# Kernel optimization log

Hardware: AMD Instinct MI355X
Metric: run time of the kernel (lower is better)

## Reference

```python
import jax, jax.numpy as jnp
import numpy as np

BN_EPS = 1e-5
N_IN, N_OUT = 200000, 400000
K, M, C_IN, C_OUT = 27, 100000, 64, 64


def setup_inputs() -> dict:
    key = jax.random.key(0)
    ks = jax.random.split(key, 4)
    x = jax.random.normal(ks[0], (N_IN, C_IN), dtype=jnp.float32)
    W = jax.random.normal(ks[1], (K, C_IN, C_OUT), dtype=jnp.float32) * 0.05
    gamma = jnp.ones((C_OUT,), dtype=jnp.float32)
    beta = jnp.zeros((C_OUT,), dtype=jnp.float32)
    in_idx = jax.random.randint(ks[2], (K, M), 0, N_IN, dtype=jnp.int32)
    out_idx = jax.random.randint(ks[3], (K, M), 0, N_OUT, dtype=jnp.int32)
    return {"x": x, "W": W, "gamma": gamma, "beta": beta,
            "in_idx": in_idx, "out_idx": out_idx, "n_out": N_OUT}


def reference(x, W, gamma, beta, in_idx, out_idx, n_out):
    # Sparse transposed conv via gather-GEMM-scatter over K kernel offsets.
    feats = x[in_idx]                               # [K, M, C_in] gather
    contrib = jnp.einsum('kmi,kio->kmo', feats, W)  # per-offset GEMM
    out = jnp.zeros((n_out, contrib.shape[-1]), dtype=x.dtype)
    out = out.at[out_idx.reshape(-1)].add(contrib.reshape(-1, contrib.shape[-1]))
    # BatchNorm (training-mode batch stats over all output points), gamma=1, beta=0 at init.
    mean = jnp.mean(out, axis=0)
    var = jnp.var(out, axis=0)
    y = (out - mean) * jax.lax.rsqrt(var + BN_EPS) * gamma + beta
    return jax.nn.relu(y)
```

## Files before the change

kernel.cpp:

```cpp
#include <hip/hip_runtime.h>
#include <hip/hip_bf16.h>

#define K_OFF 27
#define M_PTS 100000
#define C_CH 64
#define N_OUT_PTS 400000
#define BN_EPS 1e-5f
#define PTS_PER_WAVE 50

__device__ inline void pk_atomic_add_bf16(__hip_bfloat16* p, int bits) {
#if __has_builtin(__builtin_amdgcn_global_atomic_fadd_v2bf16)
    typedef short s2v __attribute__((ext_vector_type(2)));
    typedef __attribute__((address_space(1))) s2v* gp;
    s2v v;
    __builtin_memcpy(&v, &bits, 4);
    __builtin_amdgcn_global_atomic_fadd_v2bf16((gp)(unsigned long long)p, v);
#else
    asm volatile("global_atomic_pk_add_bf16 %0, %1, off"
                 :: "v"((unsigned long long)p), "v"(bits) : "memory");
#endif
}

__global__ __launch_bounds__(256, 2) void scatter_gemm(
    const float* __restrict__ x, const float* __restrict__ W,
    const int* __restrict__ in_idx, const int* __restrict__ out_idx,
    __hip_bfloat16* __restrict__ out_ws)
{
    const int k = blockIdx.y;
    const int lane = threadIdx.x & 63;
    const int wave = __builtin_amdgcn_readfirstlane(threadIdx.x >> 6);

    const float* __restrict__ Wk = W + (size_t)k * C_CH * C_CH;
    float w[C_CH];
    #pragma unroll
    for (int i = 0; i < C_CH; ++i) w[i] = Wk[i * C_CH + lane];

    const int m0 = (blockIdx.x * 4 + wave) * PTS_PER_WAVE;
    const int base = k * M_PTS + m0;

    const int li = lane < PTS_PER_WAVE ? lane : PTS_PER_WAVE - 1;
    const int vsrc = in_idx[base + li];
    const int vdst = out_idx[base + li];

    float4 u[16], v[16];
    {
        int s0 = __builtin_amdgcn_readlane(vsrc, 0);
        const float4* xr = (const float4*)(x + (size_t)s0 * C_CH);
        #pragma unroll
        for (int j = 0; j < 16; ++j) u[j] = xr[j];
        int s1 = __builtin_amdgcn_readlane(vsrc, 1);
        const float4* xs = (const float4*)(x + (size_t)s1 * C_CH);
        #pragma unroll
        for (int j = 0; j < 16; ++j) v[j] = xs[j];
    }

    const int pl = lane & 31;

    for (int p = 0; p < PTS_PER_WAVE; p += 2) {
        {
            float a0 = 0.f, a1 = 0.f;
            #pragma unroll
            for (int j = 0; j < 16; j += 2) {
                float4 t0 = u[j], t1 = u[j + 1];
                a0 = fmaf(t0.x, w[4 * j + 0], a0);
                a0 = fmaf(t0.y, w[4 * j + 1], a0);
                a0 = fmaf(t0.z, w[4 * j + 2], a0);
                a0 = fmaf(t0.w, w[4 * j + 3], a0);
                a1 = fmaf(t1.x, w[4 * j + 4], a1);
                a1 = fmaf(t1.y, w[4 * j + 5], a1);
                a1 = fmaf(t1.z, w[4 * j + 6], a1);
                a1 = fmaf(t1.w, w[4 * j + 7], a1);
            }
            float val = a0 + a1;
            int dst = __builtin_amdgcn_readlane(vdst, p);
            float lo = __shfl(val, 2 * pl);
            float hi = __shfl(val, 2 * pl + 1);
            if (lane < 32) {
                union { __hip_bfloat162 h; int i; } cv;
                cv.h = __hip_bfloat162(__float2bfloat16(lo), __float2bfloat16(hi));
                pk_atomic_add_bf16(out_ws + (size_t)dst * C_CH + 2 * lane, cv.i);
            }
        }
        {
            int pn = (p + 2 < PTS_PER_WAVE) ? p + 2 : PTS_PER_WAVE - 1;
            int sn = __builtin_amdgcn_readlane(vsrc, pn);
            const float4* xr = (const float4*)(x + (size_t)sn * C_CH);
            #pragma unroll
            for (int j = 0; j < 16; ++j) u[j] = xr[j];
        }
        {
            float a0 = 0.f, a1 = 0.f;
            #pragma unroll
            for (int j = 0; j < 16; j += 2) {
                float4 t0 = v[j], t1 = v[j + 1];
                a0 = fmaf(t0.x, w[4 * j + 0], a0);
                a0 = fmaf(t0.y, w[4 * j + 1], a0);
                a0 = fmaf(t0.z, w[4 * j + 2], a0);
                a0 = fmaf(t0.w, w[4 * j + 3], a0);
                a1 = fmaf(t1.x, w[4 * j + 4], a1);
                a1 = fmaf(t1.y, w[4 * j + 5], a1);
                a1 = fmaf(t1.z, w[4 * j + 6], a1);
                a1 = fmaf(t1.w, w[4 * j + 7], a1);
            }
            float val = a0 + a1;
            int dst = __builtin_amdgcn_readlane(vdst, p + 1);
            float lo = __shfl(val, 2 * pl);
            float hi = __shfl(val, 2 * pl + 1);
            if (lane < 32) {
                union { __hip_bfloat162 h; int i; } cv;
                cv.h = __hip_bfloat162(__float2bfloat16(lo), __float2bfloat16(hi));
                pk_atomic_add_bf16(out_ws + (size_t)dst * C_CH + 2 * lane, cv.i);
            }
        }
        {
            int pn = (p + 3 < PTS_PER_WAVE) ? p + 3 : PTS_PER_WAVE - 1;
            int sn = __builtin_amdgcn_readlane(vsrc, pn);
            const float4* xs = (const float4*)(x + (size_t)sn * C_CH);
            #pragma unroll
            for (int j = 0; j < 16; ++j) v[j] = xs[j];
        }
    }
}

__global__ __launch_bounds__(256) void bn_stats(
    const __hip_bfloat16* __restrict__ ws, float* __restrict__ stats)
{
    const uint4* in = (const uint4*)ws;
    const size_t n = (size_t)N_OUT_PTS * C_CH / 8;
    const size_t stride = (size_t)gridDim.x * blockDim.x;
    float s[8], s2[8];
    #pragma unroll
    for (int j = 0; j < 8; ++j) { s[j] = 0.f; s2[j] = 0.f; }
    for (size_t i = (size_t)blockIdx.x * blockDim.x + threadIdx.x; i < n; i += stride) {
        uint4 q = in[i];
        unsigned wds[4] = {q.x, q.y, q.z, q.w};
        #pragma unroll
        for (int j = 0; j < 4; ++j) {
            __hip_bfloat162 h = *(__hip_bfloat162*)&wds[j];
            float f0 = __low2float(h), f1 = __high2float(h);
            s[2 * j] += f0;  s2[2 * j] += f0 * f0;
            s[2 * j + 1] += f1; s2[2 * j + 1] += f1 * f1;
        }
    }
    __shared__ float sh[2][256][8];
    #pragma unroll
    for (int j = 0; j < 8; ++j) { sh[0][threadIdx.x][j] = s[j]; sh[1][threadIdx.x][j] = s2[j]; }
    __syncthreads();
    if (threadIdx.x < C_CH) {
        const int c = threadIdx.x;
        float ts = 0.f, t2 = 0.f;
        #pragma unroll
        for (int q = 0; q < 32; ++q) {
            ts += sh[0][8 * q + (c >> 3)][c & 7];
            t2 += sh[1][8 * q + (c >> 3)][c & 7];
        }
        unsafeAtomicAdd(&stats[c], ts);
        unsafeAtomicAdd(&stats[C_CH + c], t2);
    }
}

__global__ __launch_bounds__(256) void bn_apply(
    const __hip_bfloat16* __restrict__ ws, const float* __restrict__ stats,
    const float* __restrict__ gamma, const float* __restrict__ beta,
    float* __restrict__ out)
{
    const float inv_n = 1.0f / (float)N_OUT_PTS;
    const int c0 = 8 * (threadIdx.x & 7);
    float sc[8], bs[8];
    #pragma unroll
    for (int j = 0; j < 8; ++j) {
        int c = c0 + j;
        float mean = stats[c] * inv_n;
        float var = stats[C_CH + c] * inv_n - mean * mean;
        float s = gamma[c] * rsqrtf(var + BN_EPS);
        sc[j] = s;
        bs[j] = beta[c] - mean * s;
    }
    const uint4* in = (const uint4*)ws;
    float4* o4 = (float4*)out;
    const size_t n = (size_t)N_OUT_PTS * C_CH / 8;
    const size_t stride = (size_t)gridDim.x * blockDim.x;
    for (size_t i = (size_t)blockIdx.x * blockDim.x + threadIdx.x; i < n; i += stride) {
        uint4 q = in[i];
        unsigned wds[4] = {q.x, q.y, q.z, q.w};
        float f[8];
        #pragma unroll
        for (int j = 0; j < 4; ++j) {
            __hip_bfloat162 h = *(__hip_bfloat162*)&wds[j];
            f[2 * j] = __low2float(h);
            f[2 * j + 1] = __high2float(h);
        }
        float4 r0, r1;
        r0.x = fmaxf(fmaf(f[0], sc[0], bs[0]), 0.f);
        r0.y = fmaxf(fmaf(f[1], sc[1], bs[1]), 0.f);
        r0.z = fmaxf(fmaf(f[2], sc[2], bs[2]), 0.f);
        r0.w = fmaxf(fmaf(f[3], sc[3], bs[3]), 0.f);
        r1.x = fmaxf(fmaf(f[4], sc[4], bs[4]), 0.f);
        r1.y = fmaxf(fmaf(f[5], sc[5], bs[5]), 0.f);
        r1.z = fmaxf(fmaf(f[6], sc[6], bs[6]), 0.f);
        r1.w = fmaxf(fmaf(f[7], sc[7], bs[7]), 0.f);
        o4[2 * i] = r0;
        o4[2 * i + 1] = r1;
    }
}

extern "C" void kernel_launch(void* const* d_in, const int* in_sizes, int n_in,
                              void* d_out, int out_size, void* d_ws, size_t ws_size,
                              hipStream_t stream) {
    const float* x      = (const float*)d_in[0];
    const float* W      = (const float*)d_in[1];
    const float* gamma  = (const float*)d_in[2];
    const float* beta   = (const float*)d_in[3];
    const int*   in_idx = (const int*)d_in[4];
    const int*   out_idx= (const int*)d_in[5];
    float* out = (float*)d_out;

    __hip_bfloat16* out_ws = (__hip_bfloat16*)d_ws;
    const size_t acc_elems = (size_t)N_OUT_PTS * C_CH;
    float* stats = (float*)((char*)d_ws + acc_elems * sizeof(__hip_bfloat16));

    const size_t clear_bytes = acc_elems * sizeof(__hip_bfloat16) + 2 * C_CH * sizeof(float);
    (void)hipMemsetAsync(d_ws, 0, clear_bytes, stream);

    dim3 g1(M_PTS / (4 * PTS_PER_WAVE), K_OFF);
    scatter_gemm<<<g1, 256, 0, stream>>>(x, W, in_idx, out_idx, out_ws);

    bn_stats<<<2048, 256, 0, stream>>>(out_ws, stats);

    bn_apply<<<2048, 256, 0, stream>>>(out_ws, stats, gamma, beta, out);
}
```

Measured before the change: 705.3 us.

## Use bf16 MFMA tiles of 16 points with persistent grid-stride waves

Replaces the per-lane FMA dot-product scatter GEMM with 16x16x32 bf16 MFMA instructions on tiles of 16 gathered points. Weights are converted to bf16 fragments held in registers. The grid becomes a fixed 32x27 set of blocks whose waves stride over tiles, prefetching the next tile's gathered rows and indices. The goal is to cut VALU cost and register pressure so occupancy can rise. In exchange, inputs are rounded to bf16 before the multiply, which adds precision loss, and each lane now issues narrower, more scattered atomics.

```diff
diff --git a/kernel.cpp b/kernel.cpp
--- a/kernel.cpp
+++ b/kernel.cpp
@@ -6,7 +6,14 @@
 #define C_CH 64
 #define N_OUT_PTS 400000
 #define BN_EPS 1e-5f
-#define PTS_PER_WAVE 50
+
+#define TILE_PTS 16
+#define NT (M_PTS / TILE_PTS)
+#define BLKX 32
+#define WSTRIDE (BLKX * 4)
+
+typedef __attribute__((ext_vector_type(8))) short short8;
+typedef __attribute__((ext_vector_type(4))) float f32x4;
 
 __device__ inline void pk_atomic_add_bf16(__hip_bfloat16* p, int bits) {
 #if __has_builtin(__builtin_amdgcn_global_atomic_fadd_v2bf16)
@@ -21,105 +28,106 @@
 #endif
 }
 
-__global__ __launch_bounds__(256, 2) void scatter_gemm(
+__device__ inline short bf16c(float f) {
+    return __builtin_bit_cast(short, __float2bfloat16(f));
+}
+
+__device__ __attribute__((always_inline)) inline void tile_compute(
+    const float4* cur, const int* dstv, const short8 bfrag[2][4],
+    __hip_bfloat16* __restrict__ out_ws, int c)
+{
+    short8 af0, af1;
+    #pragma unroll
+    for (int j = 0; j < 4; ++j) {
+        af0[j]     = bf16c(cur[0][j]);
+        af0[j + 4] = bf16c(cur[1][j]);
+        af1[j]     = bf16c(cur[2][j]);
+        af1[j + 4] = bf16c(cur[3][j]);
+    }
+    f32x4 acc[4];
+    #pragma unroll
+    for (int tt = 0; tt < 4; ++tt) {
+        f32x4 z = {0.f, 0.f, 0.f, 0.f};
+        z       = __builtin_amdgcn_mfma_f32_16x16x32_bf16(af0, bfrag[0][tt], z, 0, 0, 0);
+        acc[tt] = __builtin_amdgcn_mfma_f32_16x16x32_bf16(af1, bfrag[1][tt], z, 0, 0, 0);
+    }
+    #pragma unroll
+    for (int e = 0; e < 4; ++e) {
+        __hip_bfloat16* rp = out_ws + (size_t)dstv[e] * C_CH + 4 * c;
+        union { __hip_bfloat162 h; int i; } p0, p1;
+        p0.h = __hip_bfloat162(__float2bfloat16(acc[0][e]), __float2bfloat16(acc[1][e]));
+        p1.h = __hip_bfloat162(__float2bfloat16(acc[2][e]), __float2bfloat16(acc[3][e]));
+        pk_atomic_add_bf16(rp, p0.i);
+        pk_atomic_add_bf16(rp + 2, p1.i);
+    }
+}
+
+__global__ __launch_bounds__(256, 4) void scatter_gemm(
     const float* __restrict__ x, const float* __restrict__ W,
     const int* __restrict__ in_idx, const int* __restrict__ out_idx,
     __hip_bfloat16* __restrict__ out_ws)
 {
     const int k = blockIdx.y;
     const int lane = threadIdx.x & 63;
-    const int wave = __builtin_amdgcn_readfirstlane(threadIdx.x >> 6);
+    const int wave = threadIdx.x >> 6;
+    const int g = lane >> 4;
+    const int c = lane & 15;
 
     const float* __restrict__ Wk = W + (size_t)k * C_CH * C_CH;
-    float w[C_CH];
-    #pragma unroll
-    for (int i = 0; i < C_CH; ++i) w[i] = Wk[i * C_CH + lane];
-
-    const int m0 = (blockIdx.x * 4 + wave) * PTS_PER_WAVE;
-    const int base = k * M_PTS + m0;
-
-    const int li = lane < PTS_PER_WAVE ? lane : PTS_PER_WAVE - 1;
-    const int vsrc = in_idx[base + li];
-    const int vdst = out_idx[base + li];
-
-    float4 u[16], v[16];
+    short8 bfrag[2][4];
+    #pragma unroll
+    for (int s = 0; s < 2; ++s) {
+        #pragma unroll
+        for (int tt = 0; tt < 4; ++tt) {
+            short8 v;
+            #pragma unroll
+            for (int j = 0; j < 8; ++j)
+                v[j] = bf16c(Wk[(size_t)(32 * s + 8 * g + j) * C_CH + 4 * c + tt]);
+            bfrag[s][tt] = v;
+        }
+    }
+
+    const int kbase = k * M_PTS;
+    const int t0 = blockIdx.x * 4 + wave;
+
+    int src_c = in_idx[kbase + t0 * TILE_PTS + c];
+    int dstv[4];
+    #pragma unroll
+    for (int e = 0; e < 4; ++e)
+        dstv[e] = out_idx[kbase + t0 * TILE_PTS + 4 * g + e];
+    float4 cur[4];
     {
-        int s0 = __builtin_amdgcn_readlane(vsrc, 0);
-        const float4* xr = (const float4*)(x + (size_t)s0 * C_CH);
-        #pragma unroll
-        for (int j = 0; j < 16; ++j) u[j] = xr[j];
-        int s1 = __builtin_amdgcn_readlane(vsrc, 1);
-        const float4* xs = (const float4*)(x + (size_t)s1 * C_CH);
-        #pragma unroll
-        for (int j = 0; j < 16; ++j) v[j] = xs[j];
-    }
-
-    const int pl = lane & 31;
-
-    for (int p = 0; p < PTS_PER_WAVE; p += 2) {
+        const float4* xr = (const float4*)x + (size_t)src_c * 16;
+        cur[0] = xr[2 * g];     cur[1] = xr[2 * g + 1];
+        cur[2] = xr[8 + 2 * g]; cur[3] = xr[8 + 2 * g + 1];
+    }
+    int src_n = (t0 + WSTRIDE < NT) ? in_idx[kbase + (t0 + WSTRIDE) * TILE_PTS + c] : 0;
+
+    int t = t0;
+    for (; t + WSTRIDE < NT; t += WSTRIDE) {
+        const int tn = t + WSTRIDE;
+        float4 nxt[4]; int dstn[4];
         {
-            float a0 = 0.f, a1 = 0.f;
+            const float4* xr = (const float4*)x + (size_t)src_n * 16;
+            nxt[0] = xr[2 * g];     nxt[1] = xr[2 * g + 1];
+            nxt[2] = xr[8 + 2 * g]; nxt[3] = xr[8 + 2 * g + 1];
             #pragma unroll
-            for (int j = 0; j < 16; j += 2) {
-                float4 t0 = u[j], t1 = u[j + 1];
-                a0 = fmaf(t0.x, w[4 * j + 0], a0);
-                a0 = fmaf(t0.y, w[4 * j + 1], a0);
-                a0 = fmaf(t0.z, w[4 * j + 2], a0);
-                a0 = fmaf(t0.w, w[4 * j + 3], a0);
-                a1 = fmaf(t1.x, w[4 * j + 4], a1);
-                a1 = fmaf(t1.y, w[4 * j + 5], a1);
-                a1 = fmaf(t1.z, w[4 * j + 6], a1);
-                a1 = fmaf(t1.w, w[4 * j + 7], a1);
-            }
-            float val = a0 + a1;
-            int dst = __builtin_amdgcn_readlane(vdst, p);
-            float lo = __shfl(val, 2 * pl);
-            float hi = __shfl(val, 2 * pl + 1);
-            if (lane < 32) {
-                union { __hip_bfloat162 h; int i; } cv;
-                cv.h = __hip_bfloat162(__float2bfloat16(lo), __float2bfloat16(hi));
-                pk_atomic_add_bf16(out_ws + (size_t)dst * C_CH + 2 * lane, cv.i);
-            }
-        }
-        {
-            int pn = (p + 2 < PTS_PER_WAVE) ? p + 2 : PTS_PER_WAVE - 1;
-            int sn = __builtin_amdgcn_readlane(vsrc, pn);
-            const float4* xr = (const float4*)(x + (size_t)sn * C_CH);
-            #pragma unroll
-            for (int j = 0; j < 16; ++j) u[j] = xr[j];
-        }
-        {
-            float a0 = 0.f, a1 = 0.f;
-            #pragma unroll
-            for (int j = 0; j < 16; j += 2) {
-                float4 t0 = v[j], t1 = v[j + 1];
-                a0 = fmaf(t0.x, w[4 * j + 0], a0);
-                a0 = fmaf(t0.y, w[4 * j + 1], a0);
-                a0 = fmaf(t0.z, w[4 * j + 2], a0);
-                a0 = fmaf(t0.w, w[4 * j + 3], a0);
-                a1 = fmaf(t1.x, w[4 * j + 4], a1);
-                a1 = fmaf(t1.y, w[4 * j + 5], a1);
-                a1 = fmaf(t1.z, w[4 * j + 6], a1);
-                a1 = fmaf(t1.w, w[4 * j + 7], a1);
-            }
-            float val = a0 + a1;
-            int dst = __builtin_amdgcn_readlane(vdst, p + 1);
-            float lo = __shfl(val, 2 * pl);
-            float hi = __shfl(val, 2 * pl + 1);
-            if (lane < 32) {
-                union { __hip_bfloat162 h; int i; } cv;
-                cv.h = __hip_bfloat162(__float2bfloat16(lo), __float2bfloat16(hi));
-                pk_atomic_add_bf16(out_ws + (size_t)dst * C_CH + 2 * lane, cv.i);
-            }
-        }
-        {
-            int pn = (p + 3 < PTS_PER_WAVE) ? p + 3 : PTS_PER_WAVE - 1;
-            int sn = __builtin_amdgcn_readlane(vsrc, pn);
-            const float4* xs = (const float4*)(x + (size_t)sn * C_CH);
-            #pragma unroll
-            for (int j = 0; j < 16; ++j) v[j] = xs[j];
-        }
-    }
+            for (int e = 0; e < 4; ++e)
+                dstn[e] = out_idx[kbase + tn * TILE_PTS + 4 * g + e];
+        }
+        const int t2 = tn + WSTRIDE;
+        const int src_2 = (t2 < NT) ? in_idx[kbase + t2 * TILE_PTS + c] : 0;
+
+        tile_compute(cur, dstv, bfrag, out_ws, c);
+
+        #pragma unroll
+        for (int j = 0; j < 4; ++j) cur[j] = nxt[j];
+        #pragma unroll
+        for (int e = 0; e < 4; ++e) dstv[e] = dstn[e];
+        src_c = src_n;
+        src_n = src_2;
+    }
+    tile_compute(cur, dstv, bfrag, out_ws, c);
 }
 
 __global__ __launch_bounds__(256) void bn_stats(
@@ -222,7 +230,7 @@
     const size_t clear_bytes = acc_elems * sizeof(__hip_bfloat16) + 2 * C_CH * sizeof(float);
     (void)hipMemsetAsync(d_ws, 0, clear_bytes, stream);
 
-    dim3 g1(M_PTS / (4 * PTS_PER_WAVE), K_OFF);
+    dim3 g1(BLKX, K_OFF);
     scatter_gemm<<<g1, 256, 0, stream>>>(x, W, in_idx, out_idx, out_ws);
 
     bn_stats<<<2048, 256, 0, stream>>>(out_ws, stats);
```

After: 766.2 us. +8.6%, slower.
